# Kernel tuning notes

Measured on AMD Instinct MI355X. Metric: run time of the kernel, lower is better.

The kernel has to match this reference:

```python
import jax, jax.numpy as jnp
import numpy as np

GROUP = 64      # int4 quantization group size
QMAX = 7.0      # symmetric int4 grid [-8, 7], scales from max/7
EPS = 1e-6      # RMSNorm epsilon


def fake_quant_int4(t, group=GROUP):
    """Symmetric per-group int4 fake-quantization along the last dim (STE)."""
    shp = t.shape
    g = t.reshape(shp[:-1] + (shp[-1] // group, group))
    s = jnp.maximum(jnp.max(jnp.abs(g), axis=-1, keepdims=True) / QMAX, 1e-8)
    q = jnp.clip(jnp.round(g / s), -8.0, 7.0) * s
    out = g + jax.lax.stop_gradient(q - g)  # straight-through
    return out.reshape(shp)


def rms_norm(x, w):
    var = jnp.mean(jnp.square(x), axis=-1, keepdims=True)
    return x * jax.lax.rsqrt(var + EPS) * w


def apply_rope(x, cos, sin):
    # x: [B,S,H,D]; cos/sin: [S, D//2]; rotate consecutive pairs (complex mult)
    xr = x.reshape(x.shape[:-1] + (x.shape[-1] // 2, 2))
    a, b = xr[..., 0], xr[..., 1]
    c = cos[None, :, None, :]
    s = sin[None, :, None, :]
    out = jnp.stack([a * c - b * s, a * s + b * c], axis=-1)
    return out.reshape(x.shape)


def setup_inputs() -> dict:
    B, S, C, OUT, R, D = 2, 4096, 3072, 9216, 32, 128
    key = jax.random.key(0)
    ks = jax.random.split(key, 6)
    x = jax.random.normal(ks[0], (B, S, C), jnp.float32)
    smooth = jax.random.uniform(ks[1], (C,), jnp.float32, minval=0.5, maxval=1.5)
    weight = jax.random.normal(ks[2], (OUT, C), jnp.float32) * 0.02
    proj_down = jax.random.normal(ks[3], (C, R), jnp.float32) * 0.02
    proj_up = jax.random.normal(ks[4], (OUT, R), jnp.float32) * 0.02
    bias = jax.random.normal(ks[5], (OUT,), jnp.float32) * 0.01
    norm_q_weight = jnp.ones((D,), jnp.float32)
    norm_k_weight = jnp.ones((D,), jnp.float32)
    half = D // 2
    inv_freq = 1.0 / (10000.0 ** (jnp.arange(half, dtype=jnp.float32) / half))
    ang = jnp.arange(S, dtype=jnp.float32)[:, None] * inv_freq[None, :]
    return {
        "x": x, "smooth": smooth, "weight": weight,
        "proj_down": proj_down, "proj_up": proj_up, "bias": bias,
        "norm_q_weight": norm_q_weight, "norm_k_weight": norm_k_weight,
        "freqs_cos": jnp.cos(ang), "freqs_sin": jnp.sin(ang),
    }


def reference(x, smooth, weight, proj_down, proj_up, bias,
              norm_q_weight, norm_k_weight, freqs_cos, freqs_sin):
    B, S, C = x.shape
    OUT = weight.shape[0]
    D = norm_q_weight.shape[0]
    H = (OUT // 3) // D
    # --- svdq_quantize_w4a4_act_fuse_lora: smooth, lora-down, int4 quantize ---
    xs = x.reshape(B * S, C) / smooth                 # smoothed activations
    lora_act = xs @ proj_down                          # [BS, R]
    xq = fake_quant_int4(xs)                           # per-token group-64 int4
    # --- svdq_gemm_w4a4: int4 GEMM + LoRA-up + bias epilogue ---
    wq = fake_quant_int4(weight)                       # per-row group-64 int4
    out = xq @ wq.T + lora_act @ proj_up.T + bias      # [BS, OUT]
    out = out.reshape(B, S, 3, H, D)                   # q,k,v concat order
    q, k, v = out[:, :, 0], out[:, :, 1], out[:, :, 2]
    # --- fused RMSNorm + RoPE epilogue on q and k ---
    q = apply_rope(rms_norm(q, norm_q_weight), freqs_cos, freqs_sin)
    k = apply_rope(rms_norm(k, norm_k_weight), freqs_cos, freqs_sin)
    return jnp.concatenate(
        [q.reshape(B, S, -1), k.reshape(B, S, -1), v.reshape(B, S, -1)], axis=-1)
```

## Files before the change

kernel.cpp:

```cpp
#include <hip/hip_runtime.h>

#define CDIM  3072
#define MROWS 8192
#define NOUT  9216
#define NTI   48

typedef __bf16 bf16x8 __attribute__((ext_vector_type(8)));
typedef float f32x4 __attribute__((ext_vector_type(4)));
typedef int i32x4 __attribute__((ext_vector_type(4)));

__device__ __forceinline__ unsigned short f2bf(float f) {
  union { float f; unsigned int u; } v; v.f = f;
  unsigned int u = v.u;
  return (unsigned short)((u + 0x7fffu + ((u >> 16) & 1u)) >> 16);
}
__device__ __forceinline__ float bfu_lo(unsigned int u) {
  union { unsigned int v; float f; } x; x.v = u << 16; return x.f;
}
__device__ __forceinline__ float bfu_hi(unsigned int u) {
  union { unsigned int v; float f; } x; x.v = u & 0xffff0000u; return x.f;
}
__device__ __forceinline__ void gld16(const void* g, void* l) {
  __builtin_amdgcn_global_load_lds(
      (const __attribute__((address_space(1))) void*)g,
      (__attribute__((address_space(3))) void*)l, 16, 0, 0);
}

#define BARRIER() asm volatile("s_barrier" ::: "memory")

template<int N> __device__ __forceinline__ void vmw() {
  if constexpr (N == 4)      asm volatile("s_waitcnt vmcnt(4)" ::: "memory");
  else if constexpr (N == 0) asm volatile("s_waitcnt vmcnt(0)" ::: "memory");
}

__device__ __forceinline__ unsigned int requant4(unsigned int u, float f) {
  const int q0 = (int)(signed char)(u & 0xff);
  const int q1 = (int)(signed char)((u >> 8) & 0xff);
  const int q2 = (int)(signed char)((u >> 16) & 0xff);
  const int q3 = (int)(signed char)(u >> 24);
  const int r0 = (int)rintf((float)q0 * f);
  const int r1 = (int)rintf((float)q1 * f);
  const int r2 = (int)rintf((float)q2 * f);
  const int r3 = (int)rintf((float)q3 * f);
  return (r0 & 0xff) | ((r1 & 0xff) << 8) | ((r2 & 0xff) << 16)
       | ((unsigned int)(r3 & 0xff) << 24);
}

__global__ __launch_bounds__(256) void k_prep(
    const float* __restrict__ wt, const float* __restrict__ pu,
    const float* __restrict__ x, const float* __restrict__ smooth,
    const float* __restrict__ pd,
    signed char* __restrict__ Bq, float* __restrict__ Sb_r,
    unsigned short* __restrict__ Blor,
    signed char* __restrict__ Aq, float* __restrict__ Sa_r,
    unsigned short* __restrict__ Alor) {
  __shared__ unsigned short xsb[4][3072];
  __shared__ float plds[4][32][33];
  __shared__ float sred[4];
  const int tid = threadIdx.x;

  if (blockIdx.x < NOUT) {
    const int row = blockIdx.x;
    unsigned int u[3]; float sl[3];
    #pragma unroll
    for (int it = 0; it < 3; ++it) {
      const int c = it * 1024 + tid * 4;
      const float4 v = *(const float4*)&wt[(size_t)row * CDIM + c];
      float am = fmaxf(fmaxf(fabsf(v.x), fabsf(v.y)), fmaxf(fabsf(v.z), fabsf(v.w)));
      #pragma unroll
      for (int off = 1; off < 16; off <<= 1) am = fmaxf(am, __shfl_xor(am, off));
      const float s = fmaxf(am / 7.0f, 1e-8f);
      union { signed char c[4]; unsigned int u; } pk;
      pk.c[0] = (signed char)(int)fminf(fmaxf(rintf(v.x / s), -8.f), 7.f);
      pk.c[1] = (signed char)(int)fminf(fmaxf(rintf(v.y / s), -8.f), 7.f);
      pk.c[2] = (signed char)(int)fminf(fmaxf(rintf(v.z / s), -8.f), 7.f);
      pk.c[3] = (signed char)(int)fminf(fmaxf(rintf(v.w / s), -8.f), 7.f);
      u[it] = pk.u; sl[it] = s;
    }
    float smax = fmaxf(fmaxf(sl[0], sl[1]), sl[2]);
    #pragma unroll
    for (int off = 16; off < 64; off <<= 1) smax = fmaxf(smax, __shfl_xor(smax, off));
    if ((tid & 63) == 0) sred[tid >> 6] = smax;
    __syncthreads();
    const float S = fmaxf(fmaxf(sred[0], sred[1]), fmaxf(sred[2], sred[3]));
    const float inv16 = 16.0f / S;
    #pragma unroll
    for (int it = 0; it < 3; ++it) {
      const int c = it * 1024 + tid * 4;
      *(unsigned int*)&Bq[(size_t)row * CDIM + c] = requant4(u[it], sl[it] * inv16);
    }
    if (tid == 0) Sb_r[row] = S * 0.0625f;
    if (tid < 32) Blor[row * 32 + tid] = f2bf(pu[row * 32 + tid]);
    return;
  }

  const int blk = blockIdx.x - NOUT;
  const int w = tid >> 6, l = tid & 63;
  const int row = blk * 4 + w;
  const float* xr = x + (size_t)row * CDIM;
  unsigned int u[12]; float sl[12];

  #pragma unroll
  for (int it = 0; it < 12; ++it) {
    const int c = it * 256 + l * 4;
    const float4 xv = *(const float4*)&xr[c];
    const float4 sm = *(const float4*)&smooth[c];
    float4 xs;
    xs.x = xv.x / sm.x; xs.y = xv.y / sm.y;
    xs.z = xv.z / sm.z; xs.w = xv.w / sm.w;
    ushort4 xb;
    xb.x = f2bf(xs.x); xb.y = f2bf(xs.y); xb.z = f2bf(xs.z); xb.w = f2bf(xs.w);
    *(ushort4*)&xsb[w][c] = xb;
    float am = fmaxf(fmaxf(fabsf(xs.x), fabsf(xs.y)), fmaxf(fabsf(xs.z), fabsf(xs.w)));
    #pragma unroll
    for (int off = 1; off < 16; off <<= 1) am = fmaxf(am, __shfl_xor(am, off));
    const float s = fmaxf(am / 7.0f, 1e-8f);
    union { signed char c[4]; unsigned int u; } pk;
    pk.c[0] = (signed char)(int)fminf(fmaxf(rintf(xs.x / s), -8.f), 7.f);
    pk.c[1] = (signed char)(int)fminf(fmaxf(rintf(xs.y / s), -8.f), 7.f);
    pk.c[2] = (signed char)(int)fminf(fmaxf(rintf(xs.z / s), -8.f), 7.f);
    pk.c[3] = (signed char)(int)fminf(fmaxf(rintf(xs.w / s), -8.f), 7.f);
    u[it] = pk.u; sl[it] = s;
  }
  float smax = sl[0];
  #pragma unroll
  for (int it = 1; it < 12; ++it) smax = fmaxf(smax, sl[it]);
  #pragma unroll
  for (int off = 16; off < 64; off <<= 1) smax = fmaxf(smax, __shfl_xor(smax, off));
  const float S = smax;
  const float inv16 = 16.0f / S;
  #pragma unroll
  for (int it = 0; it < 12; ++it) {
    const int c = it * 256 + l * 4;
    *(unsigned int*)&Aq[(size_t)row * CDIM + c] = requant4(u[it], sl[it] * inv16);
  }
  if (l == 0) Sa_r[row] = S * 0.0625f;
  __syncthreads();

  const int ch = tid >> 3, rg = tid & 7;
  float acc[4][4] = {};
  for (int i = 0; i < 48; ++i) {
    const int c = ch * 2 + i * 64;
    const float4 p0 = *(const float4*)&pd[(size_t)c * 32 + rg * 4];
    const float4 p1 = *(const float4*)&pd[(size_t)(c + 1) * 32 + rg * 4];
    #pragma unroll
    for (int r4 = 0; r4 < 4; ++r4) {
      const unsigned int uu = *(const unsigned int*)&xsb[r4][c];
      const float xa = bfu_lo(uu), xb = bfu_hi(uu);
      acc[r4][0] += xa * p0.x + xb * p1.x;
      acc[r4][1] += xa * p0.y + xb * p1.y;
      acc[r4][2] += xa * p0.z + xb * p1.z;
      acc[r4][3] += xa * p0.w + xb * p1.w;
    }
  }
  #pragma unroll
  for (int r4 = 0; r4 < 4; ++r4)
    #pragma unroll
    for (int jj = 0; jj < 4; ++jj)
      plds[r4][rg * 4 + jj][ch] = acc[r4][jj];
  __syncthreads();
  if (tid < 128) {
    const int rr = tid >> 5, r = tid & 31;
    float ssum = 0.f;
    #pragma unroll
    for (int cc = 0; cc < 32; ++cc) ssum += plds[rr][r][cc];
    Alor[(size_t)(blk * 4 + rr) * 32 + r] = f2bf(ssum);
  }
}

__global__ __launch_bounds__(256, 2) void k_gemmi8(
    const signed char* __restrict__ Aq, const signed char* __restrict__ Bq,
    const float* __restrict__ Sa_r, const float* __restrict__ Sb_r,
    const unsigned short* __restrict__ Alor, const unsigned short* __restrict__ Blor,
    const float* __restrict__ bias,
    const float* __restrict__ nqw, const float* __restrict__ nkw,
    const float* __restrict__ fcos, const float* __restrict__ fsin,
    float* __restrict__ outp) {
  __shared__ char lds[32768];
  const int tid = threadIdx.x;
  const int w = tid >> 6, l = tid & 63;
  const int wm = w >> 1, wn = w & 1;
  const int l16 = l & 15, g16 = l >> 4;
  const int xcd = blockIdx.x & 7;
  const int j = blockIdx.x >> 3;
  const int chunk = j / 36;
  const int t = j - chunk * 36;
  const int by = xcd * 8 + (chunk & 1) * 4 + t / 9;
  const int bx = (chunk >> 1) * 9 + t % 9;
  const int m0 = by * 128, n0 = bx * 128;
  const int fsb = (g16 ^ ((l16 >> 1) & 3)) << 4;
  const int rl = tid >> 2;
  const int swz = (((tid & 3) ^ ((rl >> 1) & 3)) << 4);
  const signed char* As0 = Aq + (size_t)(m0 + rl) * CDIM + swz;
  const signed char* As1 = As0 + (size_t)64 * CDIM;
  const signed char* Bs0 = Bq + (size_t)(n0 + rl) * CDIM + swz;
  const signed char* Bs1 = Bs0 + (size_t)64 * CDIM;

  i32x4 acc[4][4] = {};

  gld16(As0, lds + tid * 16);            gld16(As1, lds + 4096 + tid * 16);
  gld16(Bs0, lds + 8192 + tid * 16);     gld16(Bs1, lds + 8192 + 4096 + tid * 16);

  #pragma unroll 1
  for (int g = 0; g < NTI; ++g) {
    const int cb = (g & 1) * 16384;
    const int nb = ((g + 1) & 1) * 16384;
    if (g < NTI - 1) {
      const size_t kc = (size_t)(g + 1) * 64;
      gld16(As0 + kc, lds + nb + tid * 16);
      gld16(As1 + kc, lds + nb + 4096 + tid * 16);
      gld16(Bs0 + kc, lds + nb + 8192 + tid * 16);
      gld16(Bs1 + kc, lds + nb + 8192 + 4096 + tid * 16);
      vmw<4>();
    } else {
      vmw<0>();
    }
    BARRIER();
    i32x4 av[4], bv[4];
    #pragma unroll
    for (int mi = 0; mi < 4; ++mi)
      av[mi] = *(const i32x4*)(lds + cb + (wm * 64 + mi * 16 + l16) * 64 + fsb);
    #pragma unroll
    for (int ni = 0; ni < 4; ++ni)
      bv[ni] = *(const i32x4*)(lds + cb + 8192 + (wn * 64 + ni * 16 + l16) * 64 + fsb);
    __builtin_amdgcn_s_setprio(1);
    #pragma unroll
    for (int mi = 0; mi < 4; ++mi)
      #pragma unroll
      for (int ni = 0; ni < 4; ++ni)
        acc[mi][ni] = __builtin_amdgcn_mfma_i32_16x16x64_i8(av[mi], bv[ni], acc[mi][ni], 0, 0, 0);
    __builtin_amdgcn_s_setprio(0);
    BARRIER();
  }

  {
    const char* Al0 = (const char*)Alor + (size_t)(m0 + rl) * 64 + swz;
    const char* Bl0 = (const char*)Blor + (size_t)(n0 + rl) * 64 + swz;
    gld16(Al0, lds + tid * 16);            gld16(Al0 + 4096, lds + 4096 + tid * 16);
    gld16(Bl0, lds + 8192 + tid * 16);     gld16(Bl0 + 4096, lds + 8192 + 4096 + tid * 16);
  }

  f32x4 facc[4][4];
  float sbv[4];
  #pragma unroll
  for (int ni = 0; ni < 4; ++ni) sbv[ni] = Sb_r[n0 + wn * 64 + ni * 16 + l16];
  #pragma unroll
  for (int mi = 0; mi < 4; ++mi) {
    const f32x4 sa4 = *(const f32x4*)&Sa_r[m0 + wm * 64 + mi * 16 + g16 * 4];
    #pragma unroll
    for (int ni = 0; ni < 4; ++ni) {
      const f32x4 sab = sa4 * sbv[ni];
      facc[mi][ni] = __builtin_convertvector(acc[mi][ni], f32x4) * sab;
    }
  }

  vmw<0>();
  BARRIER();
  {
    bf16x8 bl[4];
    #pragma unroll
    for (int ni = 0; ni < 4; ++ni)
      bl[ni] = *(const bf16x8*)(lds + 8192 + (wn * 64 + ni * 16 + l16) * 64 + fsb);
    #pragma unroll
    for (int mi = 0; mi < 4; ++mi) {
      const bf16x8 al = *(const bf16x8*)(lds + (wm * 64 + mi * 16 + l16) * 64 + fsb);
      #pragma unroll
      for (int ni = 0; ni < 4; ++ni)
        facc[mi][ni] = __builtin_amdgcn_mfma_f32_16x16x32_bf16(al, bl[ni], facc[mi][ni], 0, 0, 0);
    }
  }

  float bvv[4];
  #pragma unroll
  for (int ni = 0; ni < 4; ++ni) bvv[ni] = bias[n0 + wn * 64 + ni * 16 + l16];
  #pragma unroll
  for (int mi = 0; mi < 4; ++mi)
    #pragma unroll
    for (int ni = 0; ni < 4; ++ni)
      #pragma unroll
      for (int jj = 0; jj < 4; ++jj) facc[mi][ni][jj] += bvv[ni];

  if (n0 < 6144) {
    const float* nwt = (n0 < 3072) ? nqw : nkw;
    float nw[4];
    #pragma unroll
    for (int ni = 0; ni < 4; ++ni) nw[ni] = nwt[wn * 64 + ni * 16 + l16];

    float part[4][4];
    #pragma unroll
    for (int mi = 0; mi < 4; ++mi)
      #pragma unroll
      for (int jj = 0; jj < 4; ++jj) {
        float ssum = 0.f;
        #pragma unroll
        for (int ni = 0; ni < 4; ++ni) ssum += facc[mi][ni][jj] * facc[mi][ni][jj];
        #pragma unroll
        for (int off = 1; off < 16; off <<= 1) ssum += __shfl_xor(ssum, off);
        part[mi][jj] = ssum;
      }

    __syncthreads();
    float* sq = (float*)lds;
    if (l16 == 0) {
      #pragma unroll
      for (int mi = 0; mi < 4; ++mi)
        #pragma unroll
        for (int jj = 0; jj < 4; ++jj)
          sq[(wm * 64 + mi * 16 + g16 * 4 + jj) * 2 + wn] = part[mi][jj];
    }
    __syncthreads();

    #pragma unroll
    for (int mi = 0; mi < 4; ++mi) {
      #pragma unroll
      for (int jj = 0; jj < 4; ++jj) {
        const int r128 = wm * 64 + mi * 16 + g16 * 4 + jj;
        const float other = sq[r128 * 2 + (wn ^ 1)];
        const float rinv = 1.0f / sqrtf((part[mi][jj] + other) * (1.0f / 128.0f) + 1e-6f);
        const int row = m0 + r128;
        const int sidx = row & 4095;
        #pragma unroll
        for (int ni = 0; ni < 4; ++ni) {
          const int p = wn * 32 + ni * 8 + (l16 >> 1);
          const float cv = fcos[(size_t)sidx * 64 + p];
          const float sv = fsin[(size_t)sidx * 64 + p];
          const float v = facc[mi][ni][jj] * rinv * nw[ni];
          const float o = __shfl_xor(v, 1);
          const float res = ((l & 1) == 0) ? (v * cv - o * sv) : (o * sv + v * cv);
          __builtin_nontemporal_store(res, &outp[(size_t)row * NOUT + n0 + wn * 64 + ni * 16 + l16]);
        }
      }
    }
  } else {
    #pragma unroll
    for (int ni = 0; ni < 4; ++ni) {
      const int gn = n0 + wn * 64 + ni * 16 + l16;
      #pragma unroll
      for (int mi = 0; mi < 4; ++mi) {
        const int gm = m0 + wm * 64 + mi * 16 + g16 * 4;
        #pragma unroll
        for (int jj = 0; jj < 4; ++jj)
          __builtin_nontemporal_store(facc[mi][ni][jj], &outp[(size_t)(gm + jj) * NOUT + gn]);
      }
    }
  }
}

extern "C" void kernel_launch(void* const* d_in, const int* in_sizes, int n_in,
                              void* d_out, int out_size, void* d_ws, size_t ws_size,
                              hipStream_t stream) {
  const float* x      = (const float*)d_in[0];
  const float* smooth = (const float*)d_in[1];
  const float* weight = (const float*)d_in[2];
  const float* pd     = (const float*)d_in[3];
  const float* pu     = (const float*)d_in[4];
  const float* bias   = (const float*)d_in[5];
  const float* nqw    = (const float*)d_in[6];
  const float* nkw    = (const float*)d_in[7];
  const float* fcos   = (const float*)d_in[8];
  const float* fsin   = (const float*)d_in[9];
  float* out = (float*)d_out;

  char* ws = (char*)d_ws;
  signed char* Aq   = (signed char*)ws;
  signed char* Bq   = (signed char*)(ws + 25165824);
  float* Sa_r       = (float*)(ws + 53477376);
  float* Sb_r       = (float*)(ws + 53510144);
  unsigned short* Alor = (unsigned short*)(ws + 53547008);
  unsigned short* Blor = (unsigned short*)(ws + 54071296);

  k_prep<<<dim3(NOUT + MROWS / 4), dim3(256), 0, stream>>>(
      weight, pu, x, smooth, pd, Bq, Sb_r, Blor, Aq, Sa_r, Alor);
  k_gemmi8<<<dim3(4608), dim3(256), 0, stream>>>(Aq, Bq, Sa_r, Sb_r, Alor, Blor,
                                                 bias, nqw, nkw, fcos, fsin, out);
}
```

Measured before the change: 415.9 us.

## Triple-buffer int8 GEMM main loop with one barrier per k-step

Replaces the double-buffered K loop with a three-stage LDS ring (LDS grows from 32KB to 48KB), unrolled by three. Each step issues the load two stages ahead, waits for the previous one and uses a single barrier instead of two. The LoRA operand load is folded into the final iteration so it overlaps the last MFMA step. The aim is to hide global-to-LDS latency and cut barrier stalls, at the cost of more LDS per block, which may limit occupancy.

Result: no change. 413.7 us (-0.5%).

```diff
diff --git a/kernel.cpp b/kernel.cpp
--- a/kernel.cpp
+++ b/kernel.cpp
@@ -176,7 +176,7 @@
     const float* __restrict__ nqw, const float* __restrict__ nkw,
     const float* __restrict__ fcos, const float* __restrict__ fsin,
     float* __restrict__ outp) {
-  __shared__ char lds[32768];
+  __shared__ char lds[49152];
   const int tid = threadIdx.x;
   const int w = tid >> 6, l = tid & 63;
   const int wm = w >> 1, wn = w & 1;
@@ -196,49 +196,63 @@
   const signed char* Bs0 = Bq + (size_t)(n0 + rl) * CDIM + swz;
   const signed char* Bs1 = Bs0 + (size_t)64 * CDIM;
 
+  const int aoff = (wm * 64 + l16) * 64 + fsb;
+  const int boff = 8192 + (wn * 64 + l16) * 64 + fsb;
+  char* dA0 = lds + tid * 16;
+  char* dA1 = lds + 4096 + tid * 16;
+  char* dB0 = lds + 8192 + tid * 16;
+  char* dB1 = lds + 12288 + tid * 16;
+
   i32x4 acc[4][4] = {};
-
-  gld16(As0, lds + tid * 16);            gld16(As1, lds + 4096 + tid * 16);
-  gld16(Bs0, lds + 8192 + tid * 16);     gld16(Bs1, lds + 8192 + 4096 + tid * 16);
+  int koff = 0;
+
+#define STAGE(OFF) do {                                             \
+    gld16(As0 + koff, dA0 + (OFF)); gld16(As1 + koff, dA1 + (OFF)); \
+    gld16(Bs0 + koff, dB0 + (OFF)); gld16(Bs1 + koff, dB1 + (OFF)); \
+    koff += 64; } while (0)
+
+#define STAGE_LORA(OFF) do {                                            \
+    const char* Al0 = (const char*)Alor + (size_t)(m0 + rl) * 64 + swz; \
+    const char* Bl0 = (const char*)Blor + (size_t)(n0 + rl) * 64 + swz; \
+    gld16(Al0, dA0 + (OFF)); gld16(Al0 + 4096, dA1 + (OFF));            \
+    gld16(Bl0, dB0 + (OFF)); gld16(Bl0 + 4096, dB1 + (OFF)); } while (0)
+
+#define COMPUTE(OFF) do {                                                      \
+    i32x4 av[4], bv[4];                                                        \
+    _Pragma("unroll")                                                          \
+    for (int mi = 0; mi < 4; ++mi)                                             \
+      av[mi] = *(const i32x4*)(lds + (OFF) + aoff + mi * 1024);                \
+    _Pragma("unroll")                                                          \
+    for (int ni = 0; ni < 4; ++ni)                                             \
+      bv[ni] = *(const i32x4*)(lds + (OFF) + boff + ni * 1024);                \
+    __builtin_amdgcn_s_setprio(1);                                             \
+    _Pragma("unroll")                                                          \
+    for (int mi = 0; mi < 4; ++mi)                                             \
+      _Pragma("unroll")                                                        \
+      for (int ni = 0; ni < 4; ++ni)                                           \
+        acc[mi][ni] = __builtin_amdgcn_mfma_i32_16x16x64_i8(av[mi], bv[ni],    \
+                                                            acc[mi][ni], 0, 0, 0); \
+    __builtin_amdgcn_s_setprio(0);                                             \
+  } while (0)
+
+  STAGE(0);
+  STAGE(16384);
 
   #pragma unroll 1
-  for (int g = 0; g < NTI; ++g) {
-    const int cb = (g & 1) * 16384;
-    const int nb = ((g + 1) & 1) * 16384;
-    if (g < NTI - 1) {
-      const size_t kc = (size_t)(g + 1) * 64;
-      gld16(As0 + kc, lds + nb + tid * 16);
-      gld16(As1 + kc, lds + nb + 4096 + tid * 16);
-      gld16(Bs0 + kc, lds + nb + 8192 + tid * 16);
-      gld16(Bs1 + kc, lds + nb + 8192 + 4096 + tid * 16);
-      vmw<4>();
-    } else {
-      vmw<0>();
-    }
-    BARRIER();
-    i32x4 av[4], bv[4];
-    #pragma unroll
-    for (int mi = 0; mi < 4; ++mi)
-      av[mi] = *(const i32x4*)(lds + cb + (wm * 64 + mi * 16 + l16) * 64 + fsb);
-    #pragma unroll
-    for (int ni = 0; ni < 4; ++ni)
-      bv[ni] = *(const i32x4*)(lds + cb + 8192 + (wn * 64 + ni * 16 + l16) * 64 + fsb);
-    __builtin_amdgcn_s_setprio(1);
-    #pragma unroll
-    for (int mi = 0; mi < 4; ++mi)
-      #pragma unroll
-      for (int ni = 0; ni < 4; ++ni)
-        acc[mi][ni] = __builtin_amdgcn_mfma_i32_16x16x64_i8(av[mi], bv[ni], acc[mi][ni], 0, 0, 0);
-    __builtin_amdgcn_s_setprio(0);
-    BARRIER();
-  }
-
-  {
-    const char* Al0 = (const char*)Alor + (size_t)(m0 + rl) * 64 + swz;
-    const char* Bl0 = (const char*)Blor + (size_t)(n0 + rl) * 64 + swz;
-    gld16(Al0, lds + tid * 16);            gld16(Al0 + 4096, lds + 4096 + tid * 16);
-    gld16(Bl0, lds + 8192 + tid * 16);     gld16(Bl0 + 4096, lds + 8192 + 4096 + tid * 16);
-  }
+  for (int i = 0; i < 16; ++i) {
+    vmw<4>(); BARRIER();
+    STAGE(32768);
+    COMPUTE(0);
+    vmw<4>(); BARRIER();
+    if (i < 15) STAGE(0); else STAGE_LORA(0);
+    COMPUTE(16384);
+    vmw<4>(); BARRIER();
+    if (i < 15) STAGE(16384);
+    COMPUTE(32768);
+  }
+#undef STAGE
+#undef STAGE_LORA
+#undef COMPUTE
 
   f32x4 facc[4][4];
   float sbv[4];
```
